# Performance work log

Measured on AMD Instinct MI355X. Metric: run time of the kernel, lower is better.

## Reference

```python
import jax, jax.numpy as jnp
import numpy as np

B, N, C = 32, 2048, 1024  # batch, tokens, embed_dim
LN_EPS = 1e-5


@jax.custom_vjp
def ste(x):
    # StraightThroughEstimator: hard threshold at 0.5
    return (x > 0.5).astype(x.dtype)

def _ste_fwd(x):
    return ste(x), None

def _ste_bwd(res, g):
    # torch backward: F.hardtanh(grad_output) -> clamp grad to [-1, 1]
    return (jnp.clip(g, -1.0, 1.0),)

ste.defvjp(_ste_fwd, _ste_bwd)


def layernorm(x, scale, bias, eps=LN_EPS):
    mu = jnp.mean(x, axis=-1, keepdims=True)
    var = jnp.mean(jnp.square(x - mu), axis=-1, keepdims=True)
    return (x - mu) * jax.lax.rsqrt(var + eps) * scale + bias


def setup_inputs() -> dict:
    key = jax.random.key(0)
    ks = jax.random.split(key, 8)
    u = lambda k, shape, fan_in: jax.random.uniform(
        k, shape, jnp.float32, -1.0 / np.sqrt(fan_in), 1.0 / np.sqrt(fan_in))
    return {
        "input_feature": jax.random.normal(ks[0], (B, N, C), jnp.float32),
        "noise_feature": jax.random.normal(ks[1], (1, 1, C // 2), jnp.float32),
        "prev_m": jnp.ones((B, N), jnp.float32),
        "ln_scale": jnp.ones((C,), jnp.float32),
        "ln_bias": jnp.zeros((C,), jnp.float32),
        "W_L": u(ks[2], (C, C // 2), C),        # norm1 -> L (no bias)
        "W_l1": u(ks[3], (C, C // 2), C),       # cat(C/2, C/2)=C -> C/2
        "W_l2": u(ks[4], (C // 2, C // 4), C // 2),
        "W_l3": u(ks[5], (C // 4, 1), C // 4),
    }


def reference(input_feature, noise_feature, prev_m,
              ln_scale, ln_bias, W_L, W_l1, W_l2, W_l3):
    Bn, Nn, Cd = input_feature.shape
    # gating MLP (chan_mask_gen)
    h = jax.nn.gelu(layernorm(input_feature, ln_scale, ln_bias) @ W_L,
                    approximate=False)                       # [B,N,C/2]
    nf = jnp.broadcast_to(noise_feature, (Bn, Nn, noise_feature.shape[-1]))
    h = jnp.concatenate([h, nf], axis=-1)                    # [B,N,C]
    h = jax.nn.gelu(h @ W_l1, approximate=False)             # [B,N,C/2]
    h = jax.nn.gelu(h @ W_l2, approximate=False)             # [B,N,C/4]
    prob = jax.nn.sigmoid(h @ W_l3)[..., 0]                  # [B,N]

    # training-path chanFSM: STE mask + elementwise gating
    curr_m = ste(prob * prev_m)                              # {0,1} float
    mask = curr_m.astype(jnp.int32)
    out = input_feature * curr_m[..., None]                  # [B,N,C]
    return out, mask, curr_m + 1e-10
```

## Files before the change

### kernel.cpp

```cpp
#include <hip/hip_runtime.h>
#include <hip/hip_bf16.h>
#include <math.h>

#define T_TOK 65536
#define C_DIM 1024
#define H_DIM 512
#define Q_DIM 256

typedef __attribute__((ext_vector_type(8))) short short8;
typedef __attribute__((ext_vector_type(4))) float f32x4;
typedef unsigned int u32;
typedef unsigned short u16;

#define MFMA16(a, b, c) __builtin_amdgcn_mfma_f32_16x16x32_bf16((a), (b), (c), 0, 0, 0)

#define WS_B1H 0u
#define WS_B1L (WS_B1H + 1048576u)
#define WS_B2H (WS_B1L + 1048576u)
#define WS_B2L (WS_B2H + 524288u)
#define WS_B3H (WS_B2L + 524288u)
#define WS_B3L (WS_B3H + 262144u)
#define WS_BIAS2 (WS_B3L + 262144u)
#define WS_CNT  (WS_BIAS2 + 2048u)
#define WS_LIST (WS_CNT + 256u)
#define WS_W3   (WS_LIST + 32768u)
#define WS_NEED (WS_W3 + 1024u)

#define RC_CAP 8192
#define RC_EPS 1e-3f

__device__ __forceinline__ float gelu_exact(float x) {
    return 0.5f * x * (1.0f + erff(x * 0.70710678118654752440f));
}
__device__ __forceinline__ u16 bf16_rne(float f) {
    u32 u = __float_as_uint(f);
    u32 r = u + 0x7fffu + ((u >> 16) & 1u);
    return (u16)(r >> 16);
}
__device__ __forceinline__ void split_bf16(float f, u16& hi, u16& lo) {
    u16 h = bf16_rne(f);
    float hf = __uint_as_float(((u32)h) << 16);
    hi = h;
    lo = bf16_rne(f - hf);
}

__global__ __launch_bounds__(256) void pack_kernel(const float* __restrict__ WL,
                                                   const float* __restrict__ Wl1,
                                                   const float* __restrict__ Wl2,
                                                   const float* __restrict__ w3,
                                                   unsigned char* __restrict__ ws) {
    u16* B1h = (u16*)(ws + WS_B1H); u16* B1l = (u16*)(ws + WS_B1L);
    u16* B2h = (u16*)(ws + WS_B2H); u16* B2l = (u16*)(ws + WS_B2L);
    u16* B3h = (u16*)(ws + WS_B3H); u16* B3l = (u16*)(ws + WS_B3L);
    int gid = blockIdx.x * 256 + threadIdx.x;
    if (gid == 0) *(int*)(ws + WS_CNT) = 0;
    if (gid < 256) ((float*)(ws + WS_W3))[gid] = w3[gid];
    int lane = gid & 63;
    int tg = gid >> 6;
    int kq = lane >> 4;
    int nn = lane & 15;
    if (tg < 1024) {
        int nt = tg >> 5, kt = tg & 31;
        int n = nt * 16 + nn;
        #pragma unroll
        for (int j = 0; j < 8; ++j) {
            int k = kt * 32 + kq * 8 + j;
            u16 h, l; split_bf16(WL[(size_t)k * 512 + n], h, l);
            B1h[(size_t)tg * 512 + lane * 8 + j] = h;
            B1l[(size_t)tg * 512 + lane * 8 + j] = l;
        }
    } else if (tg < 1536) {
        int t2 = tg - 1024;
        int nt = t2 >> 4, kt = t2 & 15;
        int n = nt * 16 + nn;
        #pragma unroll
        for (int j = 0; j < 8; ++j) {
            int k = kt * 32 + kq * 8 + j;
            u16 h, l; split_bf16(Wl1[(size_t)k * 512 + n], h, l);
            B2h[(size_t)t2 * 512 + lane * 8 + j] = h;
            B2l[(size_t)t2 * 512 + lane * 8 + j] = l;
        }
    } else if (tg < 1792) {
        int t3 = tg - 1536;
        int nt = t3 >> 4, kt = t3 & 15;
        int n = nt * 16 + nn;
        #pragma unroll
        for (int j = 0; j < 8; ++j) {
            int k = kt * 32 + kq * 8 + j;
            u16 h, l; split_bf16(Wl2[(size_t)k * 256 + n], h, l);
            B3h[(size_t)t3 * 512 + lane * 8 + j] = h;
            B3l[(size_t)t3 * 512 + lane * 8 + j] = l;
        }
    }
}

__global__ void bias2_kernel(const float* __restrict__ nf,
                             const float* __restrict__ Wl1,
                             float* __restrict__ bias2) {
    int n = blockIdx.x * blockDim.x + threadIdx.x;
    if (n >= H_DIM) return;
    float s = 0.0f;
    for (int j = 0; j < H_DIM; ++j)
        s = fmaf(nf[j], Wl1[(size_t)(H_DIM + j) * H_DIM + n], s);
    bias2[n] = s;
}

#define MTOK 64
#define SA_STR 136
#define SH_STR 520
#define S3_STR 260

__global__ __launch_bounds__(512, 2)
void chanFSM_mfma_kernel(const float* __restrict__ x,
                         const float* __restrict__ prev_m,
                         const float* __restrict__ gamma,
                         const float* __restrict__ beta,
                         const unsigned char* __restrict__ ws,
                         float* __restrict__ out,
                         float* __restrict__ out_mask,
                         float* __restrict__ out_curr) {
    __shared__ __align__(16) unsigned char smem[133120];
    __shared__ float sMu[MTOK], sRs[MTOK], sFlag[MTOK];
    __shared__ float sBias[H_DIM];
    __shared__ float sw3[Q_DIM];

    u16* sAh = (u16*)smem;
    u16* sAl = sAh + MTOK * SA_STR;
    u16* sHh = (u16*)smem;
    u16* sHl = sHh + MTOK * SH_STR;
    float* sH3 = (float*)smem;

    const u16* B1h = (const u16*)(ws + WS_B1H); const u16* B1l = (const u16*)(ws + WS_B1L);
    const u16* B2h = (const u16*)(ws + WS_B2H); const u16* B2l = (const u16*)(ws + WS_B2L);
    const u16* B3h = (const u16*)(ws + WS_B3H); const u16* B3l = (const u16*)(ws + WS_B3L);
    int* rc_cnt  = (int*)(ws + WS_CNT);
    int* rc_list = (int*)(ws + WS_LIST);

    const int tid = threadIdx.x;
    const int t0  = blockIdx.x * MTOK;
    const int wid = tid >> 6;
    const int ln  = tid & 63;
    const int rg  = wid & 1;
    const int cg  = wid >> 1;
    const int lm  = ln & 15;
    const int lq  = ln >> 4;

    if (tid < H_DIM) sBias[tid] = ((const float*)(ws + WS_BIAS2))[tid];
    if (tid < Q_DIM) sw3[tid] = ((const float*)(ws + WS_W3))[tid];

    for (int m = wid * 8; m < wid * 8 + 8; ++m) {
        const float* row = x + (size_t)(t0 + m) * C_DIM;
        double ds = 0.0, dq = 0.0;
        #pragma unroll
        for (int j = 0; j < 16; ++j) {
            float v = row[ln + (j << 6)];
            ds += (double)v; dq += (double)v * (double)v;
        }
        #pragma unroll
        for (int off = 32; off > 0; off >>= 1) {
            ds += __shfl_down(ds, off);
            dq += __shfl_down(dq, off);
        }
        if (ln == 0) {
            double mu = ds * (1.0 / 1024.0);
            double var = dq * (1.0 / 1024.0) - mu * mu;
            sMu[m] = (float)mu;
            sRs[m] = 1.0f / sqrtf((float)var + 1e-5f);
        }
    }

    f32x4 acc[2][8];
    #pragma unroll
    for (int rt = 0; rt < 2; ++rt)
        #pragma unroll
        for (int c = 0; c < 8; ++c) acc[rt][c] = (f32x4){0.f, 0.f, 0.f, 0.f};

    for (int chunk = 0; chunk < 8; ++chunk) {
        __syncthreads();
        #pragma unroll
        for (int i = 0; i < 4; ++i) {
            int fq = tid + (i << 9);
            int row = fq >> 5, kq = fq & 31;
            const float4 v = *(const float4*)&x[(size_t)(t0 + row) * C_DIM + chunk * 128 + kq * 4];
            float mu = sMu[row], rs = sRs[row];
            int gk = chunk * 128 + kq * 4;
            float a0 = fmaf((v.x - mu) * rs, gamma[gk],     beta[gk]);
            float a1 = fmaf((v.y - mu) * rs, gamma[gk + 1], beta[gk + 1]);
            float a2 = fmaf((v.z - mu) * rs, gamma[gk + 2], beta[gk + 2]);
            float a3 = fmaf((v.w - mu) * rs, gamma[gk + 3], beta[gk + 3]);
            u16 h0, l0, h1, l1, h2, l2, h3, l3;
            split_bf16(a0, h0, l0); split_bf16(a1, h1, l1);
            split_bf16(a2, h2, l2); split_bf16(a3, h3, l3);
            uint2 ph = make_uint2((u32)h0 | ((u32)h1 << 16), (u32)h2 | ((u32)h3 << 16));
            uint2 pl = make_uint2((u32)l0 | ((u32)l1 << 16), (u32)l2 | ((u32)l3 << 16));
            *(uint2*)&sAh[row * SA_STR + kq * 4] = ph;
            *(uint2*)&sAl[row * SA_STR + kq * 4] = pl;
        }
        __syncthreads();

        #pragma unroll
        for (int kt = 0; kt < 4; ++kt) {
            short8 ah[2], al[2];
            #pragma unroll
            for (int rt = 0; rt < 2; ++rt) {
                int row = rg * 32 + rt * 16 + lm;
                ah[rt] = *(const short8*)&sAh[row * SA_STR + kt * 32 + lq * 8];
                al[rt] = *(const short8*)&sAl[row * SA_STR + kt * 32 + lq * 8];
            }
            int ktg = chunk * 4 + kt;
            short8 bh[8], bl[8];
            #pragma unroll
            for (int c = 0; c < 8; ++c) {
                int tile = (cg * 8 + c) * 32 + ktg;
                bh[c] = *(const short8*)&B1h[(size_t)tile * 512 + ln * 8];
                bl[c] = *(const short8*)&B1l[(size_t)tile * 512 + ln * 8];
            }
            #pragma unroll
            for (int c = 0; c < 8; ++c)
                #pragma unroll
                for (int rt = 0; rt < 2; ++rt) {
                    acc[rt][c] = MFMA16(ah[rt], bh[c], acc[rt][c]);
                    acc[rt][c] = MFMA16(ah[rt], bl[c], acc[rt][c]);
                    acc[rt][c] = MFMA16(al[rt], bh[c], acc[rt][c]);
                }
        }
    }
    __syncthreads();
    #pragma unroll
    for (int rt = 0; rt < 2; ++rt)
        #pragma unroll
        for (int c = 0; c < 8; ++c) {
            int col = (cg * 8 + c) * 16 + lm;
            #pragma unroll
            for (int r = 0; r < 4; ++r) {
                int row = rg * 32 + rt * 16 + lq * 4 + r;
                u16 h, l; split_bf16(gelu_exact(acc[rt][c][r]), h, l);
                sHh[row * SH_STR + col] = h;
                sHl[row * SH_STR + col] = l;
            }
        }
    __syncthreads();

    f32x4 acc2[2][8];
    #pragma unroll
    for (int rt = 0; rt < 2; ++rt)
        #pragma unroll
        for (int c = 0; c < 8; ++c) {
            float b = sBias[(cg * 8 + c) * 16 + lm];
            acc2[rt][c] = (f32x4){b, b, b, b};
        }
    #pragma unroll 2
    for (int kt = 0; kt < 16; ++kt) {
        short8 ah[2], al[2];
        #pragma unroll
        for (int rt = 0; rt < 2; ++rt) {
            int row = rg * 32 + rt * 16 + lm;
            ah[rt] = *(const short8*)&sHh[row * SH_STR + kt * 32 + lq * 8];
            al[rt] = *(const short8*)&sHl[row * SH_STR + kt * 32 + lq * 8];
        }
        short8 bh[8], bl[8];
        #pragma unroll
        for (int c = 0; c < 8; ++c) {
            int tile = (cg * 8 + c) * 16 + kt;
            bh[c] = *(const short8*)&B2h[(size_t)tile * 512 + ln * 8];
            bl[c] = *(const short8*)&B2l[(size_t)tile * 512 + ln * 8];
        }
        #pragma unroll
        for (int c = 0; c < 8; ++c)
            #pragma unroll
            for (int rt = 0; rt < 2; ++rt) {
                acc2[rt][c] = MFMA16(ah[rt], bh[c], acc2[rt][c]);
                acc2[rt][c] = MFMA16(ah[rt], bl[c], acc2[rt][c]);
                acc2[rt][c] = MFMA16(al[rt], bh[c], acc2[rt][c]);
            }
    }
    __syncthreads();
    #pragma unroll
    for (int rt = 0; rt < 2; ++rt)
        #pragma unroll
        for (int c = 0; c < 8; ++c) {
            int col = (cg * 8 + c) * 16 + lm;
            #pragma unroll
            for (int r = 0; r < 4; ++r) {
                int row = rg * 32 + rt * 16 + lq * 4 + r;
                u16 h, l; split_bf16(gelu_exact(acc2[rt][c][r]), h, l);
                sHh[row * SH_STR + col] = h;
                sHl[row * SH_STR + col] = l;
            }
        }
    __syncthreads();

    f32x4 acc3[2][4];
    #pragma unroll
    for (int rt = 0; rt < 2; ++rt)
        #pragma unroll
        for (int c = 0; c < 4; ++c) acc3[rt][c] = (f32x4){0.f, 0.f, 0.f, 0.f};
    #pragma unroll 2
    for (int kt = 0; kt < 16; ++kt) {
        short8 ah[2], al[2];
        #pragma unroll
        for (int rt = 0; rt < 2; ++rt) {
            int row = rg * 32 + rt * 16 + lm;
            ah[rt] = *(const short8*)&sHh[row * SH_STR + kt * 32 + lq * 8];
            al[rt] = *(const short8*)&sHl[row * SH_STR + kt * 32 + lq * 8];
        }
        short8 bh[4], bl[4];
        #pragma unroll
        for (int c = 0; c < 4; ++c) {
            int tile = (cg * 4 + c) * 16 + kt;
            bh[c] = *(const short8*)&B3h[(size_t)tile * 512 + ln * 8];
            bl[c] = *(const short8*)&B3l[(size_t)tile * 512 + ln * 8];
        }
        #pragma unroll
        for (int c = 0; c < 4; ++c)
            #pragma unroll
            for (int rt = 0; rt < 2; ++rt) {
                acc3[rt][c] = MFMA16(ah[rt], bh[c], acc3[rt][c]);
                acc3[rt][c] = MFMA16(ah[rt], bl[c], acc3[rt][c]);
                acc3[rt][c] = MFMA16(al[rt], bh[c], acc3[rt][c]);
            }
    }
    __syncthreads();
    #pragma unroll
    for (int rt = 0; rt < 2; ++rt)
        #pragma unroll
        for (int c = 0; c < 4; ++c) {
            int col = (cg * 4 + c) * 16 + lm;
            #pragma unroll
            for (int r = 0; r < 4; ++r) {
                int row = rg * 32 + rt * 16 + lq * 4 + r;
                sH3[row * S3_STR + col] = gelu_exact(acc3[rt][c][r]);
            }
        }
    __syncthreads();

    for (int m = wid * 8; m < wid * 8 + 8; ++m) {
        float z = 0.0f;
        #pragma unroll
        for (int j = 0; j < 4; ++j) {
            int k = ln + (j << 6);
            z = fmaf(sH3[m * S3_STR + k], sw3[k], z);
        }
        #pragma unroll
        for (int off = 32; off > 0; off >>= 1) z += __shfl_down(z, off);
        if (ln == 0) {
            float prob = 1.0f / (1.0f + expf(-z));
            float t = prob * prev_m[t0 + m];
            float c = (t > 0.5f) ? 1.0f : 0.0f;
            sFlag[m] = c;
            out_mask[t0 + m] = c;
            out_curr[t0 + m] = (c > 0.0f) ? 1.0f : 1e-10f;
            if (fabsf(t - 0.5f) < RC_EPS) {
                int i = atomicAdd(rc_cnt, 1);
                if (i < RC_CAP) rc_list[i] = t0 + m;
            }
        }
    }
    __syncthreads();

    const float4* x4 = (const float4*)(x   + (size_t)t0 * C_DIM);
    float4*       o4 = (float4*)      (out + (size_t)t0 * C_DIM);
    #pragma unroll 4
    for (int i = 0; i < 32; ++i) {
        int idx = tid + (i << 9);
        int m = idx >> 8;
        float c = sFlag[m];
        float4 v = x4[idx];
        v.x *= c; v.y *= c; v.z *= c; v.w *= c;
        o4[idx] = v;
    }
}

__global__ __launch_bounds__(256, 2)
void recheck_kernel(const float* __restrict__ x, const float* __restrict__ prev_m,
                    const float* __restrict__ gamma, const float* __restrict__ beta,
                    const float* __restrict__ WL, const float* __restrict__ Wl1,
                    const float* __restrict__ Wl2, const float* __restrict__ w3,
                    const unsigned char* __restrict__ ws,
                    float* __restrict__ out, float* __restrict__ out_mask,
                    float* __restrict__ out_curr) {
    __shared__ __align__(16) float sx[8 * 1024];
    __shared__ __align__(16) float sh1[8 * 512];
    __shared__ __align__(16) float sh2[8 * 512];
    __shared__ __align__(16) float sh3[8 * 256];
    __shared__ double srA[8][4], srB[8][4];
    __shared__ float sMu[8], sRs[8], sFlag[8];
    __shared__ int sTok[8];

    const float* bias2 = (const float*)(ws + WS_BIAS2);
    const int* cnt = (const int*)(ws + WS_CNT);
    const int* list = (const int*)(ws + WS_LIST);
    int n = *cnt; if (n > RC_CAP) n = RC_CAP;
    if (blockIdx.x * 8 >= n) return;

    const int tid = threadIdx.x, wid = tid >> 6, ln = tid & 63;

    if (tid < 8) {
        int it = blockIdx.x * 8 + tid;
        sTok[tid] = (it < n) ? list[it] : -1;
    }
    __syncthreads();

    #pragma unroll
    for (int g = 0; g < 8; ++g) {
        int tk = sTok[g];
        if (tk >= 0) {
            const float* row = x + (size_t)tk * C_DIM;
            #pragma unroll
            for (int j = 0; j < 4; ++j)
                sx[g * 1024 + tid + (j << 8)] = row[tid + (j << 8)];
        } else {
            #pragma unroll
            for (int j = 0; j < 4; ++j)
                sx[g * 1024 + tid + (j << 8)] = 0.f;
        }
    }
    __syncthreads();

    #pragma unroll
    for (int g = 0; g < 8; ++g) {
        double ds = 0.0, dq = 0.0;
        #pragma unroll
        for (int j = 0; j < 4; ++j) {
            float v = sx[g * 1024 + tid + (j << 8)];
            ds += (double)v; dq += (double)v * (double)v;
        }
        #pragma unroll
        for (int off = 32; off > 0; off >>= 1) {
            ds += __shfl_down(ds, off); dq += __shfl_down(dq, off);
        }
        if (ln == 0) { srA[g][wid] = ds; srB[g][wid] = dq; }
    }
    __syncthreads();
    if (tid < 8) {
        double tds = srA[tid][0] + srA[tid][1] + srA[tid][2] + srA[tid][3];
        double tdq = srB[tid][0] + srB[tid][1] + srB[tid][2] + srB[tid][3];
        double mud = tds * (1.0 / 1024.0);
        sMu[tid] = (float)mud;
        sRs[tid] = 1.0f / sqrtf((float)(tdq * (1.0 / 1024.0) - mud * mud) + 1e-5f);
    }
    __syncthreads();
    #pragma unroll
    for (int g = 0; g < 8; ++g) {
        float mu = sMu[g], rs = sRs[g];
        #pragma unroll
        for (int j = 0; j < 4; ++j) {
            int k = tid + (j << 8);
            sx[g * 1024 + k] = fmaf((sx[g * 1024 + k] - mu) * rs, gamma[k], beta[k]);
        }
    }
    __syncthreads();

    {
        float acc[2][8][4];
        #pragma unroll
        for (int o = 0; o < 2; ++o)
            #pragma unroll
            for (int g = 0; g < 8; ++g)
                #pragma unroll
                for (int i = 0; i < 4; ++i) acc[o][g][i] = 0.f;
        const float2* Wp = (const float2*)WL + tid;
        #pragma unroll 2
        for (int k = 0; k < 1024; k += 4) {
            float2 w0 = Wp[(size_t)(k + 0) * 256];
            float2 w1 = Wp[(size_t)(k + 1) * 256];
            float2 w2 = Wp[(size_t)(k + 2) * 256];
            float2 w3v = Wp[(size_t)(k + 3) * 256];
            #pragma unroll
            for (int g = 0; g < 8; ++g) {
                float4 a = *(const float4*)&sx[g * 1024 + k];
                acc[0][g][0] = fmaf(a.x, w0.x, acc[0][g][0]);
                acc[1][g][0] = fmaf(a.x, w0.y, acc[1][g][0]);
                acc[0][g][1] = fmaf(a.y, w1.x, acc[0][g][1]);
                acc[1][g][1] = fmaf(a.y, w1.y, acc[1][g][1]);
                acc[0][g][2] = fmaf(a.z, w2.x, acc[0][g][2]);
                acc[1][g][2] = fmaf(a.z, w2.y, acc[1][g][2]);
                acc[0][g][3] = fmaf(a.w, w3v.x, acc[0][g][3]);
                acc[1][g][3] = fmaf(a.w, w3v.y, acc[1][g][3]);
            }
        }
        #pragma unroll
        for (int g = 0; g < 8; ++g) {
            float o0 = (acc[0][g][0] + acc[0][g][1]) + (acc[0][g][2] + acc[0][g][3]);
            float o1 = (acc[1][g][0] + acc[1][g][1]) + (acc[1][g][2] + acc[1][g][3]);
            float2 gv; gv.x = gelu_exact(o0); gv.y = gelu_exact(o1);
            *(float2*)&sh1[g * 512 + 2 * tid] = gv;
        }
    }
    __syncthreads();

    {
        float acc[2][8][4];
        float2 b2 = ((const float2*)bias2)[tid];
        #pragma unroll
        for (int g = 0; g < 8; ++g) {
            acc[0][g][0] = b2.x; acc[1][g][0] = b2.y;
            #pragma unroll
            for (int i = 1; i < 4; ++i) { acc[0][g][i] = 0.f; acc[1][g][i] = 0.f; }
        }
        const float2* Wp = (const float2*)Wl1 + tid;
        #pragma unroll 2
        for (int k = 0; k < 512; k += 4) {
            float2 w0 = Wp[(size_t)(k + 0) * 256];
            float2 w1 = Wp[(size_t)(k + 1) * 256];
            float2 w2 = Wp[(size_t)(k + 2) * 256];
            float2 w3v = Wp[(size_t)(k + 3) * 256];
            #pragma unroll
            for (int g = 0; g < 8; ++g) {
                float4 a = *(const float4*)&sh1[g * 512 + k];
                acc[0][g][0] = fmaf(a.x, w0.x, acc[0][g][0]);
                acc[1][g][0] = fmaf(a.x, w0.y, acc[1][g][0]);
                acc[0][g][1] = fmaf(a.y, w1.x, acc[0][g][1]);
                acc[1][g][1] = fmaf(a.y, w1.y, acc[1][g][1]);
                acc[0][g][2] = fmaf(a.z, w2.x, acc[0][g][2]);
                acc[1][g][2] = fmaf(a.z, w2.y, acc[1][g][2]);
                acc[0][g][3] = fmaf(a.w, w3v.x, acc[0][g][3]);
                acc[1][g][3] = fmaf(a.w, w3v.y, acc[1][g][3]);
            }
        }
        #pragma unroll
        for (int g = 0; g < 8; ++g) {
            float o0 = (acc[0][g][0] + acc[0][g][1]) + (acc[0][g][2] + acc[0][g][3]);
            float o1 = (acc[1][g][0] + acc[1][g][1]) + (acc[1][g][2] + acc[1][g][3]);
            float2 gv; gv.x = gelu_exact(o0); gv.y = gelu_exact(o1);
            *(float2*)&sh2[g * 512 + 2 * tid] = gv;
        }
    }
    __syncthreads();

    {
        float acc[8][4];
        #pragma unroll
        for (int g = 0; g < 8; ++g)
            #pragma unroll
            for (int i = 0; i < 4; ++i) acc[g][i] = 0.f;
        const float* Wp = Wl2 + tid;
        #pragma unroll 2
        for (int k = 0; k < 512; k += 4) {
            float w0 = Wp[(size_t)(k + 0) * 256];
            float w1 = Wp[(size_t)(k + 1) * 256];
            float w2 = Wp[(size_t)(k + 2) * 256];
            float w3v = Wp[(size_t)(k + 3) * 256];
            #pragma unroll
            for (int g = 0; g < 8; ++g) {
                float4 a = *(const float4*)&sh2[g * 512 + k];
                acc[g][0] = fmaf(a.x, w0, acc[g][0]);
                acc[g][1] = fmaf(a.y, w1, acc[g][1]);
                acc[g][2] = fmaf(a.z, w2, acc[g][2]);
                acc[g][3] = fmaf(a.w, w3v, acc[g][3]);
            }
        }
        #pragma unroll
        for (int g = 0; g < 8; ++g)
            sh3[g * 256 + tid] = gelu_exact((acc[g][0] + acc[g][1]) + (acc[g][2] + acc[g][3]));
    }
    __syncthreads();

    {
        float zz[8];
        float wv = w3[tid];
        #pragma unroll
        for (int g = 0; g < 8; ++g) zz[g] = sh3[g * 256 + tid] * wv;
        #pragma unroll
        for (int off = 32; off > 0; off >>= 1) {
            #pragma unroll
            for (int g = 0; g < 8; ++g) zz[g] += __shfl_down(zz[g], off);
        }
        if (ln == 0) {
            #pragma unroll
            for (int g = 0; g < 8; ++g) srA[g][wid] = (double)zz[g];
        }
    }
    __syncthreads();
    if (tid < 8) {
        int tk = sTok[tid];
        if (tk >= 0) {
            float z = (float)(srA[tid][0] + srA[tid][1] + srA[tid][2] + srA[tid][3]);
            float prob = 1.0f / (1.0f + expf(-z));
            float t = prob * prev_m[tk];
            float c = (t > 0.5f) ? 1.0f : 0.0f;
            out_mask[tk] = c;
            out_curr[tk] = (c > 0.0f) ? 1.0f : 1e-10f;
            sFlag[tid] = c;
        }
    }
    __syncthreads();
    #pragma unroll
    for (int g = 0; g < 8; ++g) {
        int tk = sTok[g];
        if (tk < 0) continue;
        float c = sFlag[g];
        float4 v = ((const float4*)(x + (size_t)tk * C_DIM))[tid];
        v.x *= c; v.y *= c; v.z *= c; v.w *= c;
        ((float4*)(out + (size_t)tk * C_DIM))[tid] = v;
    }
}

extern "C" void kernel_launch(void* const* d_in, const int* in_sizes, int n_in,
                              void* d_out, int out_size, void* d_ws, size_t ws_size,
                              hipStream_t stream) {
    const float* x      = (const float*)d_in[0];
    const float* nf     = (const float*)d_in[1];
    const float* prev_m = (const float*)d_in[2];
    const float* gamma  = (const float*)d_in[3];
    const float* beta   = (const float*)d_in[4];
    const float* WL     = (const float*)d_in[5];
    const float* Wl1    = (const float*)d_in[6];
    const float* Wl2    = (const float*)d_in[7];
    const float* w3     = (const float*)d_in[8];

    float* out      = (float*)d_out;
    float* out_mask = out + (size_t)T_TOK * C_DIM;
    float* out_curr = out_mask + T_TOK;

    unsigned char* ws = (unsigned char*)d_ws;

    pack_kernel<<<448, 256, 0, stream>>>(WL, Wl1, Wl2, w3, ws);
    bias2_kernel<<<1, 512, 0, stream>>>(nf, Wl1, (float*)(ws + WS_BIAS2));

    chanFSM_mfma_kernel<<<T_TOK / MTOK, 512, 0, stream>>>(
        x, prev_m, gamma, beta, ws, out, out_mask, out_curr);

    recheck_kernel<<<RC_CAP / 8, 256, 0, stream>>>(
        x, prev_m, gamma, beta, WL, Wl1, Wl2, w3, ws, out, out_mask, out_curr);
}
```

Baseline: 1.407 ms.

## Switch split-precision MFMA from bf16 to scaled fp16 and halve token tile

Replaces the bf16 hi/lo split emulation of fp32 GEMMs with an fp16 hi/lo split that uses scaled residuals and separate main and residual accumulators, combined at the end. The tighter fp16 split lets the recompute threshold drop from 1e-3 to 5e-5, so fewer tokens near the 0.5 threshold should need the slow fp32 recheck path. The token tile is halved to 32 rows with occupancy raised to 4 blocks per CU and LDS halved, and the fallback loops are unrolled more. The risks are fp16 range limits on activations and weights, and reduced B-fragment reuse per block.

```diff
diff --git a/kernel.cpp b/kernel.cpp
--- a/kernel.cpp
+++ b/kernel.cpp
@@ -7,12 +7,12 @@
 #define H_DIM 512
 #define Q_DIM 256
 
-typedef __attribute__((ext_vector_type(8))) short short8;
+typedef __attribute__((ext_vector_type(8))) _Float16 half8;
 typedef __attribute__((ext_vector_type(4))) float f32x4;
 typedef unsigned int u32;
 typedef unsigned short u16;
 
-#define MFMA16(a, b, c) __builtin_amdgcn_mfma_f32_16x16x32_bf16((a), (b), (c), 0, 0, 0)
+#define MFMAF(a, b, c) __builtin_amdgcn_mfma_f32_16x16x32_f16((a), (b), (c), 0, 0, 0)
 
 #define WS_B1H 0u
 #define WS_B1L (WS_B1H + 1048576u)
@@ -27,21 +27,25 @@
 #define WS_NEED (WS_W3 + 1024u)
 
 #define RC_CAP 8192
-#define RC_EPS 1e-3f
+#define RC_EPS 5e-5f
 
 __device__ __forceinline__ float gelu_exact(float x) {
     return 0.5f * x * (1.0f + erff(x * 0.70710678118654752440f));
 }
-__device__ __forceinline__ u16 bf16_rne(float f) {
-    u32 u = __float_as_uint(f);
-    u32 r = u + 0x7fffu + ((u >> 16) & 1u);
-    return (u16)(r >> 16);
-}
-__device__ __forceinline__ void split_bf16(float f, u16& hi, u16& lo) {
-    u16 h = bf16_rne(f);
-    float hf = __uint_as_float(((u32)h) << 16);
-    hi = h;
-    lo = bf16_rne(f - hf);
+__device__ __forceinline__ void split_a(float f, u16& hi, u16& lo) {
+    _Float16 h = (_Float16)f;
+    _Float16 l = (_Float16)((f - (float)h) * 2048.0f);
+    hi = __builtin_bit_cast(u16, h);
+    lo = __builtin_bit_cast(u16, l);
+}
+__device__ __forceinline__ void split_w(float f, u16& hi, u16& lo) {
+    _Float16 h = (_Float16)f;
+    _Float16 l = (_Float16)(f - (float)h);
+    hi = __builtin_bit_cast(u16, h);
+    lo = __builtin_bit_cast(u16, l);
+}
+__device__ __forceinline__ float comb(float m, float r) {
+    return fmaf(r, 4.8828125e-4f, m) * 0.03125f;
 }
 
 __global__ __launch_bounds__(256) void pack_kernel(const float* __restrict__ WL,
@@ -65,7 +69,7 @@
         #pragma unroll
         for (int j = 0; j < 8; ++j) {
             int k = kt * 32 + kq * 8 + j;
-            u16 h, l; split_bf16(WL[(size_t)k * 512 + n], h, l);
+            u16 h, l; split_w(WL[(size_t)k * 512 + n] * 32.0f, h, l);
             B1h[(size_t)tg * 512 + lane * 8 + j] = h;
             B1l[(size_t)tg * 512 + lane * 8 + j] = l;
         }
@@ -76,7 +80,7 @@
         #pragma unroll
         for (int j = 0; j < 8; ++j) {
             int k = kt * 32 + kq * 8 + j;
-            u16 h, l; split_bf16(Wl1[(size_t)k * 512 + n], h, l);
+            u16 h, l; split_w(Wl1[(size_t)k * 512 + n] * 32.0f, h, l);
             B2h[(size_t)t2 * 512 + lane * 8 + j] = h;
             B2l[(size_t)t2 * 512 + lane * 8 + j] = l;
         }
@@ -87,7 +91,7 @@
         #pragma unroll
         for (int j = 0; j < 8; ++j) {
             int k = kt * 32 + kq * 8 + j;
-            u16 h, l; split_bf16(Wl2[(size_t)k * 256 + n], h, l);
+            u16 h, l; split_w(Wl2[(size_t)k * 256 + n] * 32.0f, h, l);
             B3h[(size_t)t3 * 512 + lane * 8 + j] = h;
             B3l[(size_t)t3 * 512 + lane * 8 + j] = l;
         }
@@ -105,12 +109,12 @@
     bias2[n] = s;
 }
 
-#define MTOK 64
+#define MTOK 32
 #define SA_STR 136
 #define SH_STR 520
 #define S3_STR 260
 
-__global__ __launch_bounds__(512, 2)
+__global__ __launch_bounds__(512, 4)
 void chanFSM_mfma_kernel(const float* __restrict__ x,
                          const float* __restrict__ prev_m,
                          const float* __restrict__ gamma,
@@ -119,7 +123,7 @@
                          float* __restrict__ out,
                          float* __restrict__ out_mask,
                          float* __restrict__ out_curr) {
-    __shared__ __align__(16) unsigned char smem[133120];
+    __shared__ __align__(16) unsigned char smem[66560];
     __shared__ float sMu[MTOK], sRs[MTOK], sFlag[MTOK];
     __shared__ float sBias[H_DIM];
     __shared__ float sw3[Q_DIM];
@@ -148,7 +152,7 @@
     if (tid < H_DIM) sBias[tid] = ((const float*)(ws + WS_BIAS2))[tid];
     if (tid < Q_DIM) sw3[tid] = ((const float*)(ws + WS_W3))[tid];
 
-    for (int m = wid * 8; m < wid * 8 + 8; ++m) {
+    for (int m = wid * 4; m < wid * 4 + 4; ++m) {
         const float* row = x + (size_t)(t0 + m) * C_DIM;
         double ds = 0.0, dq = 0.0;
         #pragma unroll
@@ -169,16 +173,17 @@
         }
     }
 
-    f32x4 acc[2][8];
-    #pragma unroll
-    for (int rt = 0; rt < 2; ++rt)
-        #pragma unroll
-        for (int c = 0; c < 8; ++c) acc[rt][c] = (f32x4){0.f, 0.f, 0.f, 0.f};
+    f32x4 acc_m[8], acc_r[8];
+    #pragma unroll
+    for (int c = 0; c < 8; ++c) {
+        acc_m[c] = (f32x4){0.f, 0.f, 0.f, 0.f};
+        acc_r[c] = (f32x4){0.f, 0.f, 0.f, 0.f};
+    }
 
     for (int chunk = 0; chunk < 8; ++chunk) {
         __syncthreads();
         #pragma unroll
-        for (int i = 0; i < 4; ++i) {
+        for (int i = 0; i < 2; ++i) {
             int fq = tid + (i << 9);
             int row = fq >> 5, kq = fq & 31;
             const float4 v = *(const float4*)&x[(size_t)(t0 + row) * C_DIM + chunk * 128 + kq * 4];
@@ -189,8 +194,8 @@
             float a2 = fmaf((v.z - mu) * rs, gamma[gk + 2], beta[gk + 2]);
             float a3 = fmaf((v.w - mu) * rs, gamma[gk + 3], beta[gk + 3]);
             u16 h0, l0, h1, l1, h2, l2, h3, l3;
-            split_bf16(a0, h0, l0); split_bf16(a1, h1, l1);
-            split_bf16(a2, h2, l2); split_bf16(a3, h3, l3);
+            split_a(a0, h0, l0); split_a(a1, h1, l1);
+            split_a(a2, h2, l2); split_a(a3, h3, l3);
             uint2 ph = make_uint2((u32)h0 | ((u32)h1 << 16), (u32)h2 | ((u32)h3 << 16));
             uint2 pl = make_uint2((u32)l0 | ((u32)l1 << 16), (u32)l2 | ((u32)l3 << 16));
             *(uint2*)&sAh[row * SA_STR + kq * 4] = ph;
@@ -200,141 +205,125 @@
 
         #pragma unroll
         for (int kt = 0; kt < 4; ++kt) {
-            short8 ah[2], al[2];
-            #pragma unroll
-            for (int rt = 0; rt < 2; ++rt) {
-                int row = rg * 32 + rt * 16 + lm;
-                ah[rt] = *(const short8*)&sAh[row * SA_STR + kt * 32 + lq * 8];
-                al[rt] = *(const short8*)&sAl[row * SA_STR + kt * 32 + lq * 8];
+            int row = rg * 16 + lm;
+            half8 ah = *(const half8*)&sAh[row * SA_STR + kt * 32 + lq * 8];
+            half8 al = *(const half8*)&sAl[row * SA_STR + kt * 32 + lq * 8];
+            int ktg = chunk * 4 + kt;
+            #pragma unroll
+            for (int chf = 0; chf < 2; ++chf) {
+                half8 bh[4], bl[4];
+                #pragma unroll
+                for (int c = 0; c < 4; ++c) {
+                    int tile = (cg * 8 + chf * 4 + c) * 32 + ktg;
+                    bh[c] = *(const half8*)&B1h[(size_t)tile * 512 + ln * 8];
+                    bl[c] = *(const half8*)&B1l[(size_t)tile * 512 + ln * 8];
+                }
+                #pragma unroll
+                for (int c = 0; c < 4; ++c) {
+                    int cc = chf * 4 + c;
+                    acc_m[cc] = MFMAF(ah, bh[c], acc_m[cc]);
+                    acc_m[cc] = MFMAF(ah, bl[c], acc_m[cc]);
+                    acc_r[cc] = MFMAF(al, bh[c], acc_r[cc]);
+                }
             }
-            int ktg = chunk * 4 + kt;
-            short8 bh[8], bl[8];
-            #pragma unroll
-            for (int c = 0; c < 8; ++c) {
-                int tile = (cg * 8 + c) * 32 + ktg;
-                bh[c] = *(const short8*)&B1h[(size_t)tile * 512 + ln * 8];
-                bl[c] = *(const short8*)&B1l[(size_t)tile * 512 + ln * 8];
-            }
-            #pragma unroll
-            for (int c = 0; c < 8; ++c)
-                #pragma unroll
-                for (int rt = 0; rt < 2; ++rt) {
-                    acc[rt][c] = MFMA16(ah[rt], bh[c], acc[rt][c]);
-                    acc[rt][c] = MFMA16(ah[rt], bl[c], acc[rt][c]);
-                    acc[rt][c] = MFMA16(al[rt], bh[c], acc[rt][c]);
-                }
-        }
-    }
-    __syncthreads();
-    #pragma unroll
-    for (int rt = 0; rt < 2; ++rt)
-        #pragma unroll
-        for (int c = 0; c < 8; ++c) {
-            int col = (cg * 8 + c) * 16 + lm;
-            #pragma unroll
-            for (int r = 0; r < 4; ++r) {
-                int row = rg * 32 + rt * 16 + lq * 4 + r;
-                u16 h, l; split_bf16(gelu_exact(acc[rt][c][r]), h, l);
-                sHh[row * SH_STR + col] = h;
-                sHl[row * SH_STR + col] = l;
-            }
-        }
-    __syncthreads();
-
-    f32x4 acc2[2][8];
-    #pragma unroll
-    for (int rt = 0; rt < 2; ++rt)
-        #pragma unroll
-        for (int c = 0; c < 8; ++c) {
-            float b = sBias[(cg * 8 + c) * 16 + lm];
-            acc2[rt][c] = (f32x4){b, b, b, b};
-        }
+        }
+    }
+    __syncthreads();
+    #pragma unroll
+    for (int c = 0; c < 8; ++c) {
+        int col = (cg * 8 + c) * 16 + lm;
+        #pragma unroll
+        for (int r = 0; r < 4; ++r) {
+            int row = rg * 16 + lq * 4 + r;
+            u16 h, l; split_a(gelu_exact(comb(acc_m[c][r], acc_r[c][r])), h, l);
+            sHh[row * SH_STR + col] = h;
+            sHl[row * SH_STR + col] = l;
+        }
+    }
+    __syncthreads();
+
+    f32x4 acc2_m[8], acc2_r[8];
+    #pragma unroll
+    for (int c = 0; c < 8; ++c) {
+        float b = sBias[(cg * 8 + c) * 16 + lm] * 32.0f;
+        acc2_m[c] = (f32x4){b, b, b, b};
+        acc2_r[c] = (f32x4){0.f, 0.f, 0.f, 0.f};
+    }
     #pragma unroll 2
     for (int kt = 0; kt < 16; ++kt) {
-        short8 ah[2], al[2];
-        #pragma unroll
-        for (int rt = 0; rt < 2; ++rt) {
-            int row = rg * 32 + rt * 16 + lm;
-            ah[rt] = *(const short8*)&sHh[row * SH_STR + kt * 32 + lq * 8];
-            al[rt] = *(const short8*)&sHl[row * SH_STR + kt * 32 + lq * 8];
-        }
-        short8 bh[8], bl[8];
-        #pragma unroll
-        for (int c = 0; c < 8; ++c) {
-            int tile = (cg * 8 + c) * 16 + kt;
-            bh[c] = *(const short8*)&B2h[(size_t)tile * 512 + ln * 8];
-            bl[c] = *(const short8*)&B2l[(size_t)tile * 512 + ln * 8];
-        }
-        #pragma unroll
-        for (int c = 0; c < 8; ++c)
-            #pragma unroll
-            for (int rt = 0; rt < 2; ++rt) {
-                acc2[rt][c] = MFMA16(ah[rt], bh[c], acc2[rt][c]);
-                acc2[rt][c] = MFMA16(ah[rt], bl[c], acc2[rt][c]);
-                acc2[rt][c] = MFMA16(al[rt], bh[c], acc2[rt][c]);
+        int row = rg * 16 + lm;
+        half8 ah = *(const half8*)&sHh[row * SH_STR + kt * 32 + lq * 8];
+        half8 al = *(const half8*)&sHl[row * SH_STR + kt * 32 + lq * 8];
+        #pragma unroll
+        for (int chf = 0; chf < 2; ++chf) {
+            half8 bh[4], bl[4];
+            #pragma unroll
+            for (int c = 0; c < 4; ++c) {
+                int tile = (cg * 8 + chf * 4 + c) * 16 + kt;
+                bh[c] = *(const half8*)&B2h[(size_t)tile * 512 + ln * 8];
+                bl[c] = *(const half8*)&B2l[(size_t)tile * 512 + ln * 8];
             }
-    }
-    __syncthreads();
-    #pragma unroll
-    for (int rt = 0; rt < 2; ++rt)
-        #pragma unroll
-        for (int c = 0; c < 8; ++c) {
-            int col = (cg * 8 + c) * 16 + lm;
-            #pragma unroll
-            for (int r = 0; r < 4; ++r) {
-                int row = rg * 32 + rt * 16 + lq * 4 + r;
-                u16 h, l; split_bf16(gelu_exact(acc2[rt][c][r]), h, l);
-                sHh[row * SH_STR + col] = h;
-                sHl[row * SH_STR + col] = l;
+            #pragma unroll
+            for (int c = 0; c < 4; ++c) {
+                int cc = chf * 4 + c;
+                acc2_m[cc] = MFMAF(ah, bh[c], acc2_m[cc]);
+                acc2_m[cc] = MFMAF(ah, bl[c], acc2_m[cc]);
+                acc2_r[cc] = MFMAF(al, bh[c], acc2_r[cc]);
             }
         }
-    __syncthreads();
-
-    f32x4 acc3[2][4];
-    #pragma unroll
-    for (int rt = 0; rt < 2; ++rt)
-        #pragma unroll
-        for (int c = 0; c < 4; ++c) acc3[rt][c] = (f32x4){0.f, 0.f, 0.f, 0.f};
+    }
+    __syncthreads();
+    #pragma unroll
+    for (int c = 0; c < 8; ++c) {
+        int col = (cg * 8 + c) * 16 + lm;
+        #pragma unroll
+        for (int r = 0; r < 4; ++r) {
+            int row = rg * 16 + lq * 4 + r;
+            u16 h, l; split_a(gelu_exact(comb(acc2_m[c][r], acc2_r[c][r])), h, l);
+            sHh[row * SH_STR + col] = h;
+            sHl[row * SH_STR + col] = l;
+        }
+    }
+    __syncthreads();
+
+    f32x4 acc3_m[4], acc3_r[4];
+    #pragma unroll
+    for (int c = 0; c < 4; ++c) {
+        acc3_m[c] = (f32x4){0.f, 0.f, 0.f, 0.f};
+        acc3_r[c] = (f32x4){0.f, 0.f, 0.f, 0.f};
+    }
     #pragma unroll 2
     for (int kt = 0; kt < 16; ++kt) {
-        short8 ah[2], al[2];
-        #pragma unroll
-        for (int rt = 0; rt < 2; ++rt) {
-            int row = rg * 32 + rt * 16 + lm;
-            ah[rt] = *(const short8*)&sHh[row * SH_STR + kt * 32 + lq * 8];
-            al[rt] = *(const short8*)&sHl[row * SH_STR + kt * 32 + lq * 8];
-        }
-        short8 bh[4], bl[4];
+        int row = rg * 16 + lm;
+        half8 ah = *(const half8*)&sHh[row * SH_STR + kt * 32 + lq * 8];
+        half8 al = *(const half8*)&sHl[row * SH_STR + kt * 32 + lq * 8];
+        half8 bh[4], bl[4];
         #pragma unroll
         for (int c = 0; c < 4; ++c) {
             int tile = (cg * 4 + c) * 16 + kt;
-            bh[c] = *(const short8*)&B3h[(size_t)tile * 512 + ln * 8];
-            bl[c] = *(const short8*)&B3l[(size_t)tile * 512 + ln * 8];
-        }
-        #pragma unroll
-        for (int c = 0; c < 4; ++c)
-            #pragma unroll
-            for (int rt = 0; rt < 2; ++rt) {
-                acc3[rt][c] = MFMA16(ah[rt], bh[c], acc3[rt][c]);
-                acc3[rt][c] = MFMA16(ah[rt], bl[c], acc3[rt][c]);
-                acc3[rt][c] = MFMA16(al[rt], bh[c], acc3[rt][c]);
-            }
-    }
-    __syncthreads();
-    #pragma unroll
-    for (int rt = 0; rt < 2; ++rt)
+            bh[c] = *(const half8*)&B3h[(size_t)tile * 512 + ln * 8];
+            bl[c] = *(const half8*)&B3l[(size_t)tile * 512 + ln * 8];
+        }
         #pragma unroll
         for (int c = 0; c < 4; ++c) {
-            int col = (cg * 4 + c) * 16 + lm;
-            #pragma unroll
-            for (int r = 0; r < 4; ++r) {
-                int row = rg * 32 + rt * 16 + lq * 4 + r;
-                sH3[row * S3_STR + col] = gelu_exact(acc3[rt][c][r]);
-            }
-        }
-    __syncthreads();
-
-    for (int m = wid * 8; m < wid * 8 + 8; ++m) {
+            acc3_m[c] = MFMAF(ah, bh[c], acc3_m[c]);
+            acc3_m[c] = MFMAF(ah, bl[c], acc3_m[c]);
+            acc3_r[c] = MFMAF(al, bh[c], acc3_r[c]);
+        }
+    }
+    __syncthreads();
+    #pragma unroll
+    for (int c = 0; c < 4; ++c) {
+        int col = (cg * 4 + c) * 16 + lm;
+        #pragma unroll
+        for (int r = 0; r < 4; ++r) {
+            int row = rg * 16 + lq * 4 + r;
+            sH3[row * S3_STR + col] = gelu_exact(comb(acc3_m[c][r], acc3_r[c][r]));
+        }
+    }
+    __syncthreads();
+
+    for (int m = wid * 4; m < wid * 4 + 4; ++m) {
         float z = 0.0f;
         #pragma unroll
         for (int j = 0; j < 4; ++j) {
@@ -361,7 +350,7 @@
     const float4* x4 = (const float4*)(x   + (size_t)t0 * C_DIM);
     float4*       o4 = (float4*)      (out + (size_t)t0 * C_DIM);
     #pragma unroll 4
-    for (int i = 0; i < 32; ++i) {
+    for (int i = 0; i < 16; ++i) {
         int idx = tid + (i << 9);
         int m = idx >> 8;
         float c = sFlag[m];
@@ -460,7 +449,7 @@
                 #pragma unroll
                 for (int i = 0; i < 4; ++i) acc[o][g][i] = 0.f;
         const float2* Wp = (const float2*)WL + tid;
-        #pragma unroll 2
+        #pragma unroll 4
         for (int k = 0; k < 1024; k += 4) {
             float2 w0 = Wp[(size_t)(k + 0) * 256];
             float2 w1 = Wp[(size_t)(k + 1) * 256];
@@ -499,7 +488,7 @@
             for (int i = 1; i < 4; ++i) { acc[0][g][i] = 0.f; acc[1][g][i] = 0.f; }
         }
         const float2* Wp = (const float2*)Wl1 + tid;
-        #pragma unroll 2
+        #pragma unroll 4
         for (int k = 0; k < 512; k += 4) {
             float2 w0 = Wp[(size_t)(k + 0) * 256];
             float2 w1 = Wp[(size_t)(k + 1) * 256];
@@ -535,7 +524,7 @@
             #pragma unroll
             for (int i = 0; i < 4; ++i) acc[g][i] = 0.f;
         const float* Wp = Wl2 + tid;
-        #pragma unroll 2
+        #pragma unroll 4
         for (int k = 0; k < 512; k += 4) {
             float w0 = Wp[(size_t)(k + 0) * 256];
             float w1 = Wp[(size_t)(k + 1) * 256];
```

New measurement: 1.726 ms. 22.7% more time.

## Double-buffer LayerNorm A-tile staging and prefetch next x chunk into registers

Applied to the files above, without the earlier changes.

The first GEMM loop now keeps two shared-memory A buffers. The next chunk of x is loaded into registers before the MFMA work on the current chunk, then normalized and written into the other buffer afterward, which removes one barrier per chunk and hides global load latency. The shared-memory row strides also change to reduce bank conflicts, and the small bias kernel loop gets an unroll pragma. The cost is a slightly larger shared allocation and more registers held across the MFMA loop, which could hurt occupancy at two blocks per CU.

```diff
diff --git a/kernel.cpp b/kernel.cpp
--- a/kernel.cpp
+++ b/kernel.cpp
@@ -100,15 +100,43 @@
     int n = blockIdx.x * blockDim.x + threadIdx.x;
     if (n >= H_DIM) return;
     float s = 0.0f;
+    #pragma unroll 8
     for (int j = 0; j < H_DIM; ++j)
         s = fmaf(nf[j], Wl1[(size_t)(H_DIM + j) * H_DIM + n], s);
     bias2[n] = s;
 }
 
 #define MTOK 64
-#define SA_STR 136
-#define SH_STR 520
+#define SA_STR 140
+#define SH_STR 524
 #define S3_STR 260
+
+__device__ __forceinline__ void stage_proc(u16* __restrict__ dAh, u16* __restrict__ dAl,
+                                           const float4* xv, int tid, int chunk,
+                                           const float* __restrict__ sMu,
+                                           const float* __restrict__ sRs,
+                                           const float* __restrict__ gamma,
+                                           const float* __restrict__ beta) {
+    #pragma unroll
+    for (int i = 0; i < 4; ++i) {
+        int fq = tid + (i << 9);
+        int row = fq >> 5, kq = fq & 31;
+        float mu = sMu[row], rs = sRs[row];
+        int gk = chunk * 128 + kq * 4;
+        float4 v = xv[i];
+        float a0 = fmaf((v.x - mu) * rs, gamma[gk],     beta[gk]);
+        float a1 = fmaf((v.y - mu) * rs, gamma[gk + 1], beta[gk + 1]);
+        float a2 = fmaf((v.z - mu) * rs, gamma[gk + 2], beta[gk + 2]);
+        float a3 = fmaf((v.w - mu) * rs, gamma[gk + 3], beta[gk + 3]);
+        u16 h0, l0, h1, l1, h2, l2, h3, l3;
+        split_bf16(a0, h0, l0); split_bf16(a1, h1, l1);
+        split_bf16(a2, h2, l2); split_bf16(a3, h3, l3);
+        uint2 ph = make_uint2((u32)h0 | ((u32)h1 << 16), (u32)h2 | ((u32)h3 << 16));
+        uint2 pl = make_uint2((u32)l0 | ((u32)l1 << 16), (u32)l2 | ((u32)l3 << 16));
+        *(uint2*)&dAh[row * SA_STR + kq * 4] = ph;
+        *(uint2*)&dAl[row * SA_STR + kq * 4] = pl;
+    }
+}
 
 __global__ __launch_bounds__(512, 2)
 void chanFSM_mfma_kernel(const float* __restrict__ x,
@@ -119,13 +147,16 @@
                          float* __restrict__ out,
                          float* __restrict__ out_mask,
                          float* __restrict__ out_curr) {
-    __shared__ __align__(16) unsigned char smem[133120];
+    __shared__ __align__(16) unsigned char smem[134144];
     __shared__ float sMu[MTOK], sRs[MTOK], sFlag[MTOK];
     __shared__ float sBias[H_DIM];
     __shared__ float sw3[Q_DIM];
 
-    u16* sAh = (u16*)smem;
-    u16* sAl = sAh + MTOK * SA_STR;
+    u16* sA[4];
+    sA[0] = (u16*)smem;
+    sA[1] = sA[0] + MTOK * SA_STR;
+    sA[2] = sA[1] + MTOK * SA_STR;
+    sA[3] = sA[2] + MTOK * SA_STR;
     u16* sHh = (u16*)smem;
     u16* sHl = sHh + MTOK * SH_STR;
     float* sH3 = (float*)smem;
@@ -175,28 +206,28 @@
         #pragma unroll
         for (int c = 0; c < 8; ++c) acc[rt][c] = (f32x4){0.f, 0.f, 0.f, 0.f};
 
-    for (int chunk = 0; chunk < 8; ++chunk) {
+    float4 xv[4];
+    #pragma unroll
+    for (int i = 0; i < 4; ++i) {
+        int fq = tid + (i << 9);
+        int row = fq >> 5, kq = fq & 31;
+        xv[i] = *(const float4*)&x[(size_t)(t0 + row) * C_DIM + kq * 4];
+    }
+    __syncthreads();
+    stage_proc(sA[0], sA[1], xv, tid, 0, sMu, sRs, gamma, beta);
+
+    for (int ch = 0; ch < 8; ++ch) {
+        if (ch < 7) {
+            #pragma unroll
+            for (int i = 0; i < 4; ++i) {
+                int fq = tid + (i << 9);
+                int row = fq >> 5, kq = fq & 31;
+                xv[i] = *(const float4*)&x[(size_t)(t0 + row) * C_DIM + (ch + 1) * 128 + kq * 4];
+            }
+        }
         __syncthreads();
-        #pragma unroll
-        for (int i = 0; i < 4; ++i) {
-            int fq = tid + (i << 9);
-            int row = fq >> 5, kq = fq & 31;
-            const float4 v = *(const float4*)&x[(size_t)(t0 + row) * C_DIM + chunk * 128 + kq * 4];
-            float mu = sMu[row], rs = sRs[row];
-            int gk = chunk * 128 + kq * 4;
-            float a0 = fmaf((v.x - mu) * rs, gamma[gk],     beta[gk]);
-            float a1 = fmaf((v.y - mu) * rs, gamma[gk + 1], beta[gk + 1]);
-            float a2 = fmaf((v.z - mu) * rs, gamma[gk + 2], beta[gk + 2]);
-            float a3 = fmaf((v.w - mu) * rs, gamma[gk + 3], beta[gk + 3]);
-            u16 h0, l0, h1, l1, h2, l2, h3, l3;
-            split_bf16(a0, h0, l0); split_bf16(a1, h1, l1);
-            split_bf16(a2, h2, l2); split_bf16(a3, h3, l3);
-            uint2 ph = make_uint2((u32)h0 | ((u32)h1 << 16), (u32)h2 | ((u32)h3 << 16));
-            uint2 pl = make_uint2((u32)l0 | ((u32)l1 << 16), (u32)l2 | ((u32)l3 << 16));
-            *(uint2*)&sAh[row * SA_STR + kq * 4] = ph;
-            *(uint2*)&sAl[row * SA_STR + kq * 4] = pl;
-        }
-        __syncthreads();
+        const u16* pAh = sA[(ch & 1) * 2];
+        const u16* pAl = sA[(ch & 1) * 2 + 1];
 
         #pragma unroll
         for (int kt = 0; kt < 4; ++kt) {
@@ -204,10 +235,10 @@
             #pragma unroll
             for (int rt = 0; rt < 2; ++rt) {
                 int row = rg * 32 + rt * 16 + lm;
-                ah[rt] = *(const short8*)&sAh[row * SA_STR + kt * 32 + lq * 8];
-                al[rt] = *(const short8*)&sAl[row * SA_STR + kt * 32 + lq * 8];
-            }
-            int ktg = chunk * 4 + kt;
+                ah[rt] = *(const short8*)&pAh[row * SA_STR + kt * 32 + lq * 8];
+                al[rt] = *(const short8*)&pAl[row * SA_STR + kt * 32 + lq * 8];
+            }
+            int ktg = ch * 4 + kt;
             short8 bh[8], bl[8];
             #pragma unroll
             for (int c = 0; c < 8; ++c) {
@@ -224,6 +255,9 @@
                     acc[rt][c] = MFMA16(al[rt], bh[c], acc[rt][c]);
                 }
         }
+        if (ch < 7)
+            stage_proc(sA[((ch + 1) & 1) * 2], sA[((ch + 1) & 1) * 2 + 1],
+                       xv, tid, ch + 1, sMu, sRs, gamma, beta);
     }
     __syncthreads();
     #pragma unroll
```

Result: slower. 1.554 ms (+10.4%).
